# Optimization experiments

Hardware: AMD Instinct MI355X
Metric: run time of the kernel (lower is better)

Reference implementation:

```python
import jax, jax.numpy as jnp
import numpy as np

IN_FEATS = 128
HIDDEN = 32
OUT_CLASSES = 2
N_NODES = 100000
N_EDGES = 625000


def setup_inputs() -> dict:
    key = jax.random.key(0)
    k1, k2, k3, k4, k5, k6, k7 = jax.random.split(key, 7)
    src_nodes = jax.random.randint(k1, (N_EDGES,), 0, N_NODES, dtype=jnp.int64 if jax.config.jax_enable_x64 else jnp.int32)
    dst_nodes = jax.random.randint(k2, (N_EDGES,), 0, N_NODES, dtype=jnp.int64 if jax.config.jax_enable_x64 else jnp.int32)
    node_embed = jax.random.normal(k3, (N_NODES, IN_FEATS), dtype=jnp.float32)
    # Linear params (torch nn.Linear default init: U(-1/sqrt(fan_in), 1/sqrt(fan_in)))
    lim1 = 1.0 / np.sqrt(2 * IN_FEATS)
    W1 = jax.random.uniform(k4, (HIDDEN, 2 * IN_FEATS), jnp.float32, -lim1, lim1)
    b1 = jax.random.uniform(k5, (HIDDEN,), jnp.float32, -lim1, lim1)
    lim2 = 1.0 / np.sqrt(HIDDEN)
    W2 = jax.random.uniform(k6, (OUT_CLASSES, HIDDEN), jnp.float32, -lim2, lim2)
    b2 = jax.random.uniform(k7, (OUT_CLASSES,), jnp.float32, -lim2, lim2)
    return {"src_nodes": src_nodes, "dst_nodes": dst_nodes, "node_embed": node_embed,
            "W1": W1, "b1": b1, "W2": W2, "b2": b2}


def reference(src_nodes, dst_nodes, node_embed, W1, b1, W2, b2):
    # Gather endpoint embeddings: [E, F] each
    src_e = node_embed[src_nodes]
    dst_e = node_embed[dst_nodes]
    # Avoid materializing the concat explicitly in the GEMM by splitting W1:
    # fc1(cat([s, d])) == s @ W1[:, :F].T + d @ W1[:, F:].T + b1
    W1s, W1d = W1[:, :IN_FEATS], W1[:, IN_FEATS:]
    h = jax.nn.relu(src_e @ W1s.T + dst_e @ W1d.T + b1)  # [E, 32]
    logits = h @ W2.T + b2  # [E, out_classes]
    return logits
```

## Files before the change

### kernel.cpp

```cpp
#include <hip/hip_runtime.h>
#include <hip/hip_bf16.h>

#define IN_FEATS 128
#define HIDDEN 32

typedef short v8s __attribute__((ext_vector_type(8)));
typedef unsigned short u16x8 __attribute__((ext_vector_type(8)));
typedef float v4f __attribute__((ext_vector_type(4)));

__device__ __forceinline__ short hw_f2bf(float x) {
    __hip_bfloat16 b = __float2bfloat16(x);
    return *reinterpret_cast<short*>(&b);
}
__device__ __forceinline__ float bf2f_raw(unsigned short b) {
    union { float f; unsigned int u; } v; v.u = ((unsigned int)b) << 16;
    return v.f;
}

__global__ __launch_bounds__(256, 4) void precompute_P_mfma(
    const float* __restrict__ embed,
    const float* __restrict__ W1,
    const float* __restrict__ b1,
    unsigned short* __restrict__ P,
    int n_nodes)
{
    __shared__ unsigned short sBhi[8192];
    __shared__ unsigned short sBlo[8192];

    const int t    = threadIdx.x;
    const int lane = t & 63;
    const int wave = t >> 6;

#pragma unroll
    for (int g0 = 0; g0 < 1024; g0 += 256) {
        const int g   = g0 + t;
        const int gl  = g & 63;
        const int ks  = (g >> 6) & 3;
        const int nb  = g >> 8;
        const int u   = nb * 16 + (gl & 15);
        const int k0  = ks * 32 + ((gl >> 4) & 3) * 8;
        const float* wp = W1 + (u & 31) * (2 * IN_FEATS) + (u >> 5) * IN_FEATS + k0;
        const float4 x0 = *reinterpret_cast<const float4*>(wp);
        const float4 x1 = *reinterpret_cast<const float4*>(wp + 4);
        const float xs[8] = {x0.x, x0.y, x0.z, x0.w, x1.x, x1.y, x1.z, x1.w};
        v8s h, l;
#pragma unroll
        for (int j = 0; j < 8; ++j) {
            const short hb = hw_f2bf(xs[j]);
            h[j] = hb;
            l[j] = hw_f2bf(xs[j] - bf2f_raw((unsigned short)hb));
        }
        *reinterpret_cast<v8s*>(sBhi + g * 8) = h;
        *reinterpret_cast<v8s*>(sBlo + g * 8) = l;
    }
    __syncthreads();

    const float bias_nb0 = b1[lane & 15];
    const float bias_nb1 = b1[16 + (lane & 15)];

    const int last = n_nodes - 1;
    const int grp  = lane >> 4;

#pragma unroll
    for (int sub = 0; sub < 2; ++sub) {
        const int node0 = blockIdx.x * 128 + wave * 32 + sub * 16;
        if (node0 >= n_nodes) break;
        const int row = min(node0 + (lane & 15), last);

        v8s ahi[4], alo[4];
#pragma unroll
        for (int ks = 0; ks < 4; ++ks) {
            const float* ap = embed + (size_t)row * IN_FEATS + ks * 32 + grp * 8;
            const float4 x0 = *reinterpret_cast<const float4*>(ap);
            const float4 x1 = *reinterpret_cast<const float4*>(ap + 4);
            const float xs[8] = {x0.x, x0.y, x0.z, x0.w, x1.x, x1.y, x1.z, x1.w};
            v8s h, l;
#pragma unroll
            for (int j = 0; j < 8; ++j) {
                const short hb = hw_f2bf(xs[j]);
                h[j] = hb;
                l[j] = hw_f2bf(xs[j] - bf2f_raw((unsigned short)hb));
            }
            ahi[ks] = h;
            alo[ks] = l;
        }

#pragma unroll
        for (int nb = 0; nb < 4; ++nb) {
            v8s bhi[4], blo[4];
#pragma unroll
            for (int ks = 0; ks < 4; ++ks) {
                const int fi = ((nb * 4 + ks) * 64 + lane) * 8;
                bhi[ks] = *reinterpret_cast<const v8s*>(sBhi + fi);
                blo[ks] = *reinterpret_cast<const v8s*>(sBlo + fi);
            }
            v4f acc = {0.f, 0.f, 0.f, 0.f};
#pragma unroll
            for (int ks = 0; ks < 4; ++ks) {
                acc = __builtin_amdgcn_mfma_f32_16x16x32_bf16(ahi[ks], bhi[ks], acc, 0, 0, 0);
                acc = __builtin_amdgcn_mfma_f32_16x16x32_bf16(ahi[ks], blo[ks], acc, 0, 0, 0);
                acc = __builtin_amdgcn_mfma_f32_16x16x32_bf16(alo[ks], bhi[ks], acc, 0, 0, 0);
            }
            const float bias = (nb == 0) ? bias_nb0 : (nb == 1) ? bias_nb1 : 0.f;
            const int u = nb * 16 + (lane & 15);
#pragma unroll
            for (int r = 0; r < 4; ++r) {
                const int n = node0 + grp * 4 + r;
                if (n < n_nodes)
                    P[(size_t)n * 64 + u] = (unsigned short)hw_f2bf(acc[r] + bias);
            }
        }
    }
}

__global__ __launch_bounds__(256) void edge_classify_bf16(
    const int* __restrict__ src,
    const int* __restrict__ dst,
    const unsigned short* __restrict__ P,
    const float* __restrict__ W2,
    const float* __restrict__ b2,
    float* __restrict__ out,
    int n_edges)
{
    const int t   = threadIdx.x;
    const int q   = t & 3;
    const int qid = t >> 2;
    const int e0  = blockIdx.x * 256 + qid;
    if (e0 >= n_edges) return;

    int se[4], de[4];
#pragma unroll
    for (int k = 0; k < 4; ++k) {
        const int e  = e0 + k * 64;
        const int ec = (e < n_edges) ? e : e0;
        se[k] = src[ec];
        de[k] = dst[ec];
    }

    u16x8 ps[4], pd[4];
#pragma unroll
    for (int k = 0; k < 4; ++k) {
        ps[k] = *reinterpret_cast<const u16x8*>(P + (size_t)se[k] * 64 + q * 8);
        pd[k] = *reinterpret_cast<const u16x8*>(P + (size_t)de[k] * 64 + 32 + q * 8);
    }

    const float4 w0a = *reinterpret_cast<const float4*>(W2 + q * 8);
    const float4 w0b = *reinterpret_cast<const float4*>(W2 + q * 8 + 4);
    const float4 w1a = *reinterpret_cast<const float4*>(W2 + HIDDEN + q * 8);
    const float4 w1b = *reinterpret_cast<const float4*>(W2 + HIDDEN + q * 8 + 4);
    const float ww0[8] = {w0a.x, w0a.y, w0a.z, w0a.w, w0b.x, w0b.y, w0b.z, w0b.w};
    const float ww1[8] = {w1a.x, w1a.y, w1a.z, w1a.w, w1b.x, w1b.y, w1b.z, w1b.w};

    float l0[4] = {0.f, 0.f, 0.f, 0.f};
    float l1[4] = {0.f, 0.f, 0.f, 0.f};
#pragma unroll
    for (int k = 0; k < 4; ++k) {
#pragma unroll
        for (int j = 0; j < 8; ++j) {
            float h = bf2f_raw(ps[k][j]) + bf2f_raw(pd[k][j]);
            h = fmaxf(h, 0.f);
            l0[k] = fmaf(h, ww0[j], l0[k]);
            l1[k] = fmaf(h, ww1[j], l1[k]);
        }
    }
#pragma unroll
    for (int k = 0; k < 4; ++k) {
        l0[k] += __shfl_xor(l0[k], 1); l0[k] += __shfl_xor(l0[k], 2);
        l1[k] += __shfl_xor(l1[k], 1); l1[k] += __shfl_xor(l1[k], 2);
    }
    if (q == 0) {
        const float bias0 = b2[0], bias1 = b2[1];
#pragma unroll
        for (int k = 0; k < 4; ++k) {
            const int e = e0 + k * 64;
            if (e < n_edges)
                *reinterpret_cast<float2*>(out + (size_t)e * 2) =
                    make_float2(l0[k] + bias0, l1[k] + bias1);
        }
    }
}

__global__ __launch_bounds__(256) void edge_direct(
    const int* __restrict__ src, const int* __restrict__ dst,
    const float* __restrict__ embed,
    const float* __restrict__ W1, const float* __restrict__ b1,
    const float* __restrict__ W2, const float* __restrict__ b2,
    float* __restrict__ out, int n_edges)
{
    const int e = blockIdx.x * 256 + threadIdx.x;
    if (e >= n_edges) return;
    const int s = src[e], d = dst[e];
    const float* se = embed + (size_t)s * IN_FEATS;
    const float* de = embed + (size_t)d * IN_FEATS;

    float acc[HIDDEN];
#pragma unroll
    for (int hh = 0; hh < HIDDEN; ++hh) acc[hh] = b1[hh];

    for (int c = 0; c < 4; ++c) {
        float es[32], ed[32];
#pragma unroll
        for (int q = 0; q < 8; ++q) {
            const float4 v = *reinterpret_cast<const float4*>(se + c * 32 + q * 4);
            es[q*4+0] = v.x; es[q*4+1] = v.y; es[q*4+2] = v.z; es[q*4+3] = v.w;
            const float4 u = *reinterpret_cast<const float4*>(de + c * 32 + q * 4);
            ed[q*4+0] = u.x; ed[q*4+1] = u.y; ed[q*4+2] = u.z; ed[q*4+3] = u.w;
        }
#pragma unroll
        for (int hh = 0; hh < HIDDEN; ++hh) {
            float acch = acc[hh];
#pragma unroll
            for (int k = 0; k < 32; ++k) {
                acch = fmaf(es[k], W1[hh * 256 + c * 32 + k], acch);
                acch = fmaf(ed[k], W1[hh * 256 + 128 + c * 32 + k], acch);
            }
            acc[hh] = acch;
        }
    }

    float l0 = b2[0], l1 = b2[1];
#pragma unroll
    for (int hh = 0; hh < HIDDEN; ++hh) {
        const float hv = fmaxf(acc[hh], 0.f);
        l0 = fmaf(hv, W2[hh], l0);
        l1 = fmaf(hv, W2[HIDDEN + hh], l1);
    }
    *reinterpret_cast<float2*>(out + (size_t)e * 2) = make_float2(l0, l1);
}

extern "C" void kernel_launch(void* const* d_in, const int* in_sizes, int n_in,
                              void* d_out, int out_size, void* d_ws, size_t ws_size,
                              hipStream_t stream)
{
    const int*   src = (const int*)d_in[0];
    const int*   dst = (const int*)d_in[1];
    const float* emb = (const float*)d_in[2];
    const float* W1  = (const float*)d_in[3];
    const float* b1  = (const float*)d_in[4];
    const float* W2  = (const float*)d_in[5];
    const float* b2  = (const float*)d_in[6];
    float* out = (float*)d_out;

    const int n_edges = in_sizes[0];
    const int n_nodes = in_sizes[2] / IN_FEATS;

    const size_t p_bytes = (size_t)n_nodes * 64 * sizeof(unsigned short);

    if (ws_size >= p_bytes) {
        unsigned short* P = (unsigned short*)d_ws;
        const int nb_nodes = (n_nodes + 127) / 128;
        precompute_P_mfma<<<nb_nodes, 256, 0, stream>>>(emb, W1, b1, P, n_nodes);
        const int nb_edges = (n_edges + 255) / 256;
        edge_classify_bf16<<<nb_edges, 256, 0, stream>>>(src, dst, P, W2, b2, out, n_edges);
    } else {
        const int nb_edges = (n_edges + 255) / 256;
        edge_direct<<<nb_edges, 256, 0, stream>>>(src, dst, emb, W1, b1, W2, b2, out, n_edges);
    }
}
```

Measured before the change: 41.41 us.

## Drop lo-part of embeddings in P precompute and vectorize P stores

Removes the bf16 low-part split of the node embeddings, so the precompute runs two MFMAs per k-step instead of three and skips half the conversion work. It also permutes the output column mapping of the weight tile so that each lane owns four consecutive P columns, which allows packed ushort4 stores in place of scalar 16-bit stores, with bias loaded as a float4. In exchange, P is computed with reduced precision on the activation side, which may increase error in the final logits.

```diff
diff --git a/kernel.cpp b/kernel.cpp
--- a/kernel.cpp
+++ b/kernel.cpp
@@ -37,7 +37,7 @@
         const int gl  = g & 63;
         const int ks  = (g >> 6) & 3;
         const int nb  = g >> 8;
-        const int u   = nb * 16 + (gl & 15);
+        const int u   = (gl & 15) * 4 + nb;
         const int k0  = ks * 32 + ((gl >> 4) & 3) * 8;
         const float* wp = W1 + (u & 31) * (2 * IN_FEATS) + (u >> 5) * IN_FEATS + k0;
         const float4 x0 = *reinterpret_cast<const float4*>(wp);
@@ -55,8 +55,12 @@
     }
     __syncthreads();
 
-    const float bias_nb0 = b1[lane & 15];
-    const float bias_nb1 = b1[16 + (lane & 15)];
+    v4f bias_vec = {0.f, 0.f, 0.f, 0.f};
+    if ((lane & 15) < 8) {
+        const float4 bv = *reinterpret_cast<const float4*>(b1 + (lane & 15) * 4);
+        bias_vec[0] = bv.x; bias_vec[1] = bv.y;
+        bias_vec[2] = bv.z; bias_vec[3] = bv.w;
+    }
 
     const int last = n_nodes - 1;
     const int grp  = lane >> 4;
@@ -67,47 +71,45 @@
         if (node0 >= n_nodes) break;
         const int row = min(node0 + (lane & 15), last);
 
-        v8s ahi[4], alo[4];
+        v8s ahi[4];
 #pragma unroll
         for (int ks = 0; ks < 4; ++ks) {
             const float* ap = embed + (size_t)row * IN_FEATS + ks * 32 + grp * 8;
             const float4 x0 = *reinterpret_cast<const float4*>(ap);
             const float4 x1 = *reinterpret_cast<const float4*>(ap + 4);
             const float xs[8] = {x0.x, x0.y, x0.z, x0.w, x1.x, x1.y, x1.z, x1.w};
-            v8s h, l;
-#pragma unroll
-            for (int j = 0; j < 8; ++j) {
-                const short hb = hw_f2bf(xs[j]);
-                h[j] = hb;
-                l[j] = hw_f2bf(xs[j] - bf2f_raw((unsigned short)hb));
-            }
+            v8s h;
+#pragma unroll
+            for (int j = 0; j < 8; ++j)
+                h[j] = hw_f2bf(xs[j]);
             ahi[ks] = h;
-            alo[ks] = l;
-        }
-
+        }
+
+        v4f acc[4];
 #pragma unroll
         for (int nb = 0; nb < 4; ++nb) {
-            v8s bhi[4], blo[4];
+            v4f a = {0.f, 0.f, 0.f, 0.f};
 #pragma unroll
             for (int ks = 0; ks < 4; ++ks) {
                 const int fi = ((nb * 4 + ks) * 64 + lane) * 8;
-                bhi[ks] = *reinterpret_cast<const v8s*>(sBhi + fi);
-                blo[ks] = *reinterpret_cast<const v8s*>(sBlo + fi);
+                const v8s bhi = *reinterpret_cast<const v8s*>(sBhi + fi);
+                const v8s blo = *reinterpret_cast<const v8s*>(sBlo + fi);
+                a = __builtin_amdgcn_mfma_f32_16x16x32_bf16(ahi[ks], bhi, a, 0, 0, 0);
+                a = __builtin_amdgcn_mfma_f32_16x16x32_bf16(ahi[ks], blo, a, 0, 0, 0);
             }
-            v4f acc = {0.f, 0.f, 0.f, 0.f};
-#pragma unroll
-            for (int ks = 0; ks < 4; ++ks) {
-                acc = __builtin_amdgcn_mfma_f32_16x16x32_bf16(ahi[ks], bhi[ks], acc, 0, 0, 0);
-                acc = __builtin_amdgcn_mfma_f32_16x16x32_bf16(ahi[ks], blo[ks], acc, 0, 0, 0);
-                acc = __builtin_amdgcn_mfma_f32_16x16x32_bf16(alo[ks], bhi[ks], acc, 0, 0, 0);
-            }
-            const float bias = (nb == 0) ? bias_nb0 : (nb == 1) ? bias_nb1 : 0.f;
-            const int u = nb * 16 + (lane & 15);
-#pragma unroll
-            for (int r = 0; r < 4; ++r) {
-                const int n = node0 + grp * 4 + r;
-                if (n < n_nodes)
-                    P[(size_t)n * 64 + u] = (unsigned short)hw_f2bf(acc[r] + bias);
+            acc[nb] = a;
+        }
+
+#pragma unroll
+        for (int r = 0; r < 4; ++r) {
+            const int n = node0 + grp * 4 + r;
+            if (n < n_nodes) {
+                ushort4 v;
+                v.x = (unsigned short)hw_f2bf(acc[0][r] + bias_vec[0]);
+                v.y = (unsigned short)hw_f2bf(acc[1][r] + bias_vec[1]);
+                v.z = (unsigned short)hw_f2bf(acc[2][r] + bias_vec[2]);
+                v.w = (unsigned short)hw_f2bf(acc[3][r] + bias_vec[3]);
+                *reinterpret_cast<ushort4*>(P + (size_t)n * 64 + (lane & 15) * 4) = v;
             }
         }
     }
```

New measurement: 39.49 us. -4.6%, faster.
